# Kernel tuning notes

Measured on AMD Instinct MI355X. Metric: run time of the kernel, lower is better.

Reference implementation:

```python
import jax, jax.numpy as jnp
import numpy as np

N, M, D_IN, D_OUT = 100000, 1024, 64, 64


def setup_inputs() -> dict:
    key = jax.random.key(0)
    ks = jax.random.split(key, 8)
    # kaiming_uniform_ bound for fan_in = D_IN: sqrt(6 / fan_in) with a=sqrt(5) default? torch's
    # kaiming_uniform_ default (a=0) gives bound = sqrt(6/fan_in); exact init is irrelevant for math.
    bound = float(np.sqrt(6.0 / D_IN))
    return {
        "x": jax.random.normal(ks[0], (N, D_IN), dtype=jnp.float32),
        "neighbors": jax.random.normal(ks[1], (M, D_IN), dtype=jnp.float32),
        "Wq": jax.random.uniform(ks[2], (D_OUT, D_IN), jnp.float32, -bound, bound),
        "bq": jnp.zeros((D_OUT,), jnp.float32),
        "Wk": jax.random.uniform(ks[3], (D_OUT, D_IN), jnp.float32, -bound, bound),
        "bk": jnp.zeros((D_OUT,), jnp.float32),
        "Wv": jax.random.uniform(ks[4], (D_OUT, D_IN), jnp.float32, -bound, bound),
        "bv": jnp.zeros((D_OUT,), jnp.float32),
    }


def reference(x, neighbors, Wq, bq, Wk, bk, Wv, bv):
    # q: [N, D_OUT], k: [M, D_OUT]
    q = x @ Wq.T + bq
    k = neighbors @ Wk.T + bk
    # scores: [N, M] -- same math as sum(q[:,None,:] * k[None,:,:], axis=2) but via GEMM
    scores = q @ k.T
    attn = jax.nn.softmax(scores, axis=1)
    # attn @ neighbors: [N, D_IN], then value projection -> [N, D_OUT]
    agg = attn @ neighbors
    return agg @ Wv.T + bv
```

## Files before the change

### kernel.cpp

```cpp
#include <hip/hip_runtime.h>


#define N_ROWS 100000
#define VT_STRIDE 1040

typedef __attribute__((ext_vector_type(8))) _Float16 half8;
typedef __attribute__((ext_vector_type(4))) float    f32x4;

#define MFMA16(a,b,c) __builtin_amdgcn_mfma_f32_16x16x32_f16((a),(b),(c),0,0,0)

static __device__ __forceinline__ f32x4 zero4() {
    f32x4 v = {0.f, 0.f, 0.f, 0.f};
    return v;
}

__global__ __launch_bounds__(256)
void prep_kernel(const float* __restrict__ nb, const float* __restrict__ Wq,
                 const float* __restrict__ bq, const float* __restrict__ Wk,
                 unsigned short* __restrict__ Gh, unsigned short* __restrict__ Gl,
                 float* __restrict__ uW, unsigned short* __restrict__ Kp,
                 unsigned short* __restrict__ VTp)
{
    __shared__ __align__(16) float sm[8192];
    const int tid = threadIdx.x;
    if (blockIdx.x == 0) {
        const float4* wk4 = (const float4*)Wk;
        const float4* wq4 = (const float4*)Wq;
        float4* dk = (float4*)sm;
        float4* dq = (float4*)(sm + 4096);
        #pragma unroll
        for (int u = 0; u < 4; u++) {
            dk[u * 256 + tid] = wk4[u * 256 + tid];
            dq[u * 256 + tid] = wq4[u * 256 + tid];
        }
        __syncthreads();
        const int e2 = tid & 63, e1g = (tid >> 6) * 16;
        float g[16];
        #pragma unroll
        for (int q = 0; q < 16; q++) g[q] = 0.f;
        for (int w = 0; w < 64; w++) {
            float kv = sm[w * 64 + e2];
            const float* wqp = sm + 4096 + w * 64 + e1g;
            #pragma unroll
            for (int q = 0; q < 16; q++) g[q] = fmaf(wqp[q], kv, g[q]);
        }
        union { half8 h; uint4 u; } ph0, pl0, ph1, pl1;
        #pragma unroll
        for (int i = 0; i < 8; i++) {
            _Float16 h0 = (_Float16)g[i];
            ph0.h[i] = h0; pl0.h[i] = (_Float16)(g[i] - (float)h0);
            _Float16 h1 = (_Float16)g[8 + i];
            ph1.h[i] = h1; pl1.h[i] = (_Float16)(g[8 + i] - (float)h1);
        }
        *(uint4*)(Gh + e2 * 72 + e1g)     = ph0.u;
        *(uint4*)(Gh + e2 * 72 + e1g + 8) = ph1.u;
        *(uint4*)(Gl + e2 * 72 + e1g)     = pl0.u;
        *(uint4*)(Gl + e2 * 72 + e1g + 8) = pl1.u;
        if (tid < 64) {
            float uu = 0.f;
            for (int w = 0; w < 64; w++) uu = fmaf(bq[w], sm[w * 64 + tid], uu);
            uW[tid] = uu;
        }
    } else {
        const int j0 = (blockIdx.x - 1) * 64;
        const int jr = tid >> 2;
        const int c0 = (tid & 3) * 16;
        const float* np = nb + (size_t)(j0 + jr) * 64 + c0;
        float a[16];
        #pragma unroll
        for (int u = 0; u < 4; u++) *(float4*)(a + 4 * u) = *(const float4*)(np + 4 * u);
        const int pr = (jr & ~31) | (((jr >> 2) & 1) << 4) | (((jr >> 3) & 3) << 2) | (jr & 3);
        union { half8 h; uint4 u; } pk0, pk1;
        #pragma unroll
        for (int i = 0; i < 8; i++) { pk0.h[i] = (_Float16)a[i]; pk1.h[i] = (_Float16)a[8 + i]; }
        *(uint4*)(Kp + (size_t)(j0 + pr) * 72 + c0)     = pk0.u;
        *(uint4*)(Kp + (size_t)(j0 + pr) * 72 + c0 + 8) = pk1.u;
        #pragma unroll
        for (int i = 0; i < 16; i++) sm[jr * 65 + c0 + i] = a[i];
        __syncthreads();
        const int d   = tid >> 2;
        const int jc0 = (tid & 3) * 16;
        union { half8 h; uint4 u; } pv0, pv1;
        #pragma unroll
        for (int i = 0; i < 8; i++) {
            pv0.h[i] = (_Float16)sm[(jc0 + i) * 65 + d];
            pv1.h[i] = (_Float16)sm[(jc0 + 8 + i) * 65 + d];
        }
        *(uint4*)(VTp + (size_t)d * VT_STRIDE + j0 + jc0)     = pv0.u;
        *(uint4*)(VTp + (size_t)d * VT_STRIDE + j0 + jc0 + 8) = pv1.u;
    }
}

static __device__ __forceinline__ void flash_step(
    int jb, int jn, int c, int Q,
    const unsigned short* __restrict__ Kp, const unsigned short* __restrict__ VTp,
    const half8 (&ck0)[2], const half8 (&ck1)[2],
    half8 (&nk0)[2], half8 (&nk1)[2],
    const half8 (&qh)[2][2], const half8 (&ql)[2][2],
    f32x4 (&acc)[2][4], float (&mrow)[2], float (&lrow)[2])
{
    half8 vA[4];
    #pragma unroll
    for (int dt = 0; dt < 4; dt++)
        vA[dt] = *(const half8*)(VTp + (size_t)(dt * 16 + c) * VT_STRIDE + jb + Q * 8);
    #pragma unroll
    for (int t = 0; t < 2; t++) {
        const unsigned short* kp = Kp + (size_t)(jn + 16 * t + c) * 72;
        nk0[t] = *(const half8*)(kp + Q * 8);
        nk1[t] = *(const half8*)(kp + 32 + Q * 8);
    }
    f32x4 S[2][2];
    #pragma unroll
    for (int t = 0; t < 2; t++)
        #pragma unroll
        for (int qt = 0; qt < 2; qt++) {
            f32x4 s = MFMA16(ck0[t], qh[qt][0], zero4());
            s = MFMA16(ck1[t], qh[qt][1], s);
            s = MFMA16(ck0[t], ql[qt][0], s);
            s = MFMA16(ck1[t], ql[qt][1], s);
            S[t][qt] = s;
        }
    half8 pB[2];
    #pragma unroll
    for (int qt = 0; qt < 2; qt++) {
        float pmax = fmaxf(fmaxf(fmaxf(S[0][qt][0], S[0][qt][1]),
                                 fmaxf(S[0][qt][2], S[0][qt][3])),
                           fmaxf(fmaxf(S[1][qt][0], S[1][qt][1]),
                                 fmaxf(S[1][qt][2], S[1][qt][3])));
        if (__any(pmax > mrow[qt] + 8.f)) {
            float cm = pmax;
            cm = fmaxf(cm, __shfl_xor(cm, 16));
            cm = fmaxf(cm, __shfl_xor(cm, 32));
            const float mn = fmaxf(mrow[qt], cm);
            const float sc = __expf(mrow[qt] - mn);
            mrow[qt] = mn;
            lrow[qt] *= sc;
            #pragma unroll
            for (int dt = 0; dt < 4; dt++)
                #pragma unroll
                for (int r = 0; r < 4; r++) acc[qt][dt][r] *= sc;
        }
        const float mref = mrow[qt];
        float p[8]; float ps = 0.f;
        #pragma unroll
        for (int r = 0; r < 4; r++) { p[r] = __expf(S[0][qt][r] - mref); ps += p[r]; }
        #pragma unroll
        for (int r = 0; r < 4; r++) { p[4 + r] = __expf(S[1][qt][r] - mref); ps += p[4 + r]; }
        lrow[qt] += ps;
        #pragma unroll
        for (int i = 0; i < 8; i++) pB[qt][i] = (_Float16)p[i];
    }
    #pragma unroll
    for (int dt = 0; dt < 4; dt++) {
        acc[0][dt] = MFMA16(vA[dt], pB[0], acc[0][dt]);
        acc[1][dt] = MFMA16(vA[dt], pB[1], acc[1][dt]);
    }
}

__global__ __launch_bounds__(64, 3)
void attn_kernel(const float* __restrict__ x,
                 const unsigned short* __restrict__ Gh,
                 const unsigned short* __restrict__ Gl,
                 const float* __restrict__ uW,
                 const unsigned short* __restrict__ Kp,
                 const unsigned short* __restrict__ VTp,
                 const float* __restrict__ Wv,
                 const float* __restrict__ bv,
                 float* __restrict__ out)
{
    __shared__ __align__(16) float slice[1088];
    const int lane = threadIdx.x & 63;
    const int Q    = lane >> 4;
    const int c    = lane & 15;
    const int rbase = blockIdx.x * 32;

    half8 qh[2][2], ql[2][2];
    #pragma unroll
    for (int rt = 0; rt < 2; rt++) {
        int row = rbase + rt * 16 + c;
        if (row > N_ROWS - 1) row = N_ROWS - 1;
        half8 xh[2], xl[2];
        #pragma unroll
        for (int ks = 0; ks < 2; ks++) {
            const float* xp = x + (size_t)row * 64 + ks * 32 + Q * 8;
            float a[8];
            *(float4*)a       = *(const float4*)xp;
            *(float4*)(a + 4) = *(const float4*)(xp + 4);
            #pragma unroll
            for (int i = 0; i < 8; i++) {
                _Float16 h = (_Float16)a[i];
                xh[ks][i] = h;
                xl[ks][i] = (_Float16)(a[i] - (float)h);
            }
        }
        #pragma unroll
        for (int mt = 0; mt < 4; mt++) {
            f32x4 Cm = zero4();
            #pragma unroll
            for (int ks = 0; ks < 2; ks++) {
                half8 gh = *(const half8*)(Gh + (mt * 16 + c) * 72 + ks * 32 + Q * 8);
                half8 gl = *(const half8*)(Gl + (mt * 16 + c) * 72 + ks * 32 + Q * 8);
                Cm = MFMA16(gh, xh[ks], Cm);
                Cm = MFMA16(gh, xl[ks], Cm);
                Cm = MFMA16(gl, xh[ks], Cm);
            }
            *(f32x4*)(slice + c * 68 + mt * 16 + 4 * Q) = Cm;
        }
        __builtin_amdgcn_s_waitcnt(0);
        #pragma unroll
        for (int ks = 0; ks < 2; ks++) {
            const float* qp = slice + c * 68 + ks * 32 + Q * 8;
            const float* up = uW + ks * 32 + Q * 8;
            #pragma unroll
            for (int i = 0; i < 8; i++) {
                float val = qp[i] + up[i];
                _Float16 h = (_Float16)val;
                qh[rt][ks][i] = h;
                ql[rt][ks][i] = (_Float16)(val - (float)h);
            }
        }
        __builtin_amdgcn_s_waitcnt(0);
    }

    f32x4 acc[2][4];
    #pragma unroll
    for (int qt = 0; qt < 2; qt++)
        #pragma unroll
        for (int dt = 0; dt < 4; dt++) acc[qt][dt] = zero4();
    float mrow[2] = { -3.0e38f, -3.0e38f };
    float lrow[2] = { 0.f, 0.f };

    half8 ka0[2], ka1[2], kb0[2], kb1[2];
    #pragma unroll
    for (int t = 0; t < 2; t++) {
        const unsigned short* kp = Kp + (size_t)(16 * t + c) * 72;
        ka0[t] = *(const half8*)(kp + Q * 8);
        ka1[t] = *(const half8*)(kp + 32 + Q * 8);
    }
    #pragma unroll 1
    for (int jj = 0; jj < 16; jj++) {
        const int jb = jj * 64;
        flash_step(jb,      jb + 32, c, Q, Kp, VTp, ka0, ka1, kb0, kb1, qh, ql, acc, mrow, lrow);
        const int jn2 = (jb + 64 < 1024) ? jb + 64 : jb + 32;
        flash_step(jb + 32, jn2,     c, Q, Kp, VTp, kb0, kb1, ka0, ka1, qh, ql, acc, mrow, lrow);
    }

    #pragma unroll
    for (int qt = 0; qt < 2; qt++) {
        float l = lrow[qt];
        l += __shfl_xor(l, 16);
        l += __shfl_xor(l, 32);
        const float rl = 1.f / l;
        #pragma unroll
        for (int dt = 0; dt < 4; dt++)
            #pragma unroll
            for (int r = 0; r < 4; r++) acc[qt][dt][r] *= rl;
    }
    half8 wf[4][2];
    #pragma unroll
    for (int mt = 0; mt < 4; mt++)
        #pragma unroll
        for (int ks = 0; ks < 2; ks++) {
            const float* wp = Wv + (size_t)(mt * 16 + c) * 64 + ks * 32 + Q * 8;
            #pragma unroll
            for (int i = 0; i < 8; i++) wf[mt][ks][i] = (_Float16)wp[i];
        }
    const int srcA = 32 * (Q & 1) + c;
    const int srcB = srcA + 16;
    const bool hi = (Q >> 1) & 1;
    f32x4 o[2][4];
    #pragma unroll
    for (int qt = 0; qt < 2; qt++) {
        half8 pe[2];
        #pragma unroll
        for (int ks = 0; ks < 2; ks++) {
            #pragma unroll
            for (int r = 0; r < 4; r++) {
                float a0 = __shfl(acc[qt][2 * ks + 0][r], srcA);
                float a1 = __shfl(acc[qt][2 * ks + 1][r], srcA);
                float b0 = __shfl(acc[qt][2 * ks + 0][r], srcB);
                float b1 = __shfl(acc[qt][2 * ks + 1][r], srcB);
                pe[ks][r]     = (_Float16)(hi ? a1 : a0);
                pe[ks][4 + r] = (_Float16)(hi ? b1 : b0);
            }
        }
        #pragma unroll
        for (int mt = 0; mt < 4; mt++) {
            f32x4 t = MFMA16(wf[mt][0], pe[0], zero4());
            o[qt][mt] = MFMA16(wf[mt][1], pe[1], t);
        }
    }
    float4 bf[4];
    #pragma unroll
    for (int mt = 0; mt < 4; mt++) bf[mt] = *(const float4*)(bv + mt * 16 + 4 * Q);
    #pragma unroll
    for (int qt = 0; qt < 2; qt++) {
        const int row = rbase + qt * 16 + c;
        if (row < N_ROWS) {
            #pragma unroll
            for (int mt = 0; mt < 4; mt++) {
                float4 vv = make_float4(o[qt][mt][0] + bf[mt].x, o[qt][mt][1] + bf[mt].y,
                                        o[qt][mt][2] + bf[mt].z, o[qt][mt][3] + bf[mt].w);
                *(float4*)(out + (size_t)row * 64 + mt * 16 + 4 * Q) = vv;
            }
        }
    }
}

extern "C" void kernel_launch(void* const* d_in, const int* in_sizes, int n_in,
                              void* d_out, int out_size, void* d_ws, size_t ws_size,
                              hipStream_t stream)
{
    const float* x  = (const float*)d_in[0];
    const float* nb = (const float*)d_in[1];
    const float* Wq = (const float*)d_in[2];
    const float* bq = (const float*)d_in[3];
    const float* Wk = (const float*)d_in[4];
    const float* Wv = (const float*)d_in[6];
    const float* bv = (const float*)d_in[7];
    float* out = (float*)d_out;

    char* ws = (char*)d_ws;
    unsigned short* Gh  = (unsigned short*)(ws);
    unsigned short* Gl  = (unsigned short*)(ws + 9216);
    float*          uW  = (float*)(ws + 18432);
    unsigned short* Kp  = (unsigned short*)(ws + 18688);
    unsigned short* VTp = (unsigned short*)(ws + 166144);

    prep_kernel<<<17, 256, 0, stream>>>(nb, Wq, bq, Wk, Gh, Gl, uW, Kp, VTp);
    const int grid = N_ROWS / 32;
    attn_kernel<<<grid, 64, 0, stream>>>(x, Gh, Gl, uW, Kp, VTp, Wv, bv, out);
}
```

Baseline: 161.7 us.

## Pre-swizzle K, V and G into MFMA fragment order and prefetch V one tile ahead

After: 149.2 us. 1.08x faster.

```diff
diff --git a/kernel.cpp b/kernel.cpp
--- a/kernel.cpp
+++ b/kernel.cpp
@@ -2,7 +2,6 @@
 
 
 #define N_ROWS 100000
-#define VT_STRIDE 1040
 
 typedef __attribute__((ext_vector_type(8))) _Float16 half8;
 typedef __attribute__((ext_vector_type(4))) float    f32x4;
@@ -17,9 +16,9 @@
 __global__ __launch_bounds__(256)
 void prep_kernel(const float* __restrict__ nb, const float* __restrict__ Wq,
                  const float* __restrict__ bq, const float* __restrict__ Wk,
-                 unsigned short* __restrict__ Gh, unsigned short* __restrict__ Gl,
-                 float* __restrict__ uW, unsigned short* __restrict__ Kp,
-                 unsigned short* __restrict__ VTp)
+                 unsigned short* __restrict__ GFh, unsigned short* __restrict__ GFl,
+                 float* __restrict__ uW, unsigned short* __restrict__ KF,
+                 unsigned short* __restrict__ VF)
 {
     __shared__ __align__(16) float sm[8192];
     const int tid = threadIdx.x;
@@ -52,10 +51,13 @@
             _Float16 h1 = (_Float16)g[8 + i];
             ph1.h[i] = h1; pl1.h[i] = (_Float16)(g[8 + i] - (float)h1);
         }
-        *(uint4*)(Gh + e2 * 72 + e1g)     = ph0.u;
-        *(uint4*)(Gh + e2 * 72 + e1g + 8) = ph1.u;
-        *(uint4*)(Gl + e2 * 72 + e1g)     = pl0.u;
-        *(uint4*)(Gl + e2 * 72 + e1g + 8) = pl1.u;
+        const int mt = e2 >> 4, cc = e2 & 15;
+        const int ks = tid >> 7, Q0 = 2 * ((tid >> 6) & 1);
+        const int f  = mt * 2 + ks;
+        *(uint4*)(GFh + (f * 64 + Q0 * 16 + cc) * 8)       = ph0.u;
+        *(uint4*)(GFh + (f * 64 + (Q0 + 1) * 16 + cc) * 8) = ph1.u;
+        *(uint4*)(GFl + (f * 64 + Q0 * 16 + cc) * 8)       = pl0.u;
+        *(uint4*)(GFl + (f * 64 + (Q0 + 1) * 16 + cc) * 8) = pl1.u;
         if (tid < 64) {
             float uu = 0.f;
             for (int w = 0; w < 64; w++) uu = fmaf(bq[w], sm[w * 64 + tid], uu);
@@ -63,61 +65,69 @@
         }
     } else {
         const int j0 = (blockIdx.x - 1) * 64;
-        const int jr = tid >> 2;
-        const int c0 = (tid & 3) * 16;
-        const float* np = nb + (size_t)(j0 + jr) * 64 + c0;
-        float a[16];
-        #pragma unroll
-        for (int u = 0; u < 4; u++) *(float4*)(a + 4 * u) = *(const float4*)(np + 4 * u);
-        const int pr = (jr & ~31) | (((jr >> 2) & 1) << 4) | (((jr >> 3) & 3) << 2) | (jr & 3);
-        union { half8 h; uint4 u; } pk0, pk1;
-        #pragma unroll
-        for (int i = 0; i < 8; i++) { pk0.h[i] = (_Float16)a[i]; pk1.h[i] = (_Float16)a[8 + i]; }
-        *(uint4*)(Kp + (size_t)(j0 + pr) * 72 + c0)     = pk0.u;
-        *(uint4*)(Kp + (size_t)(j0 + pr) * 72 + c0 + 8) = pk1.u;
-        #pragma unroll
-        for (int i = 0; i < 16; i++) sm[jr * 65 + c0 + i] = a[i];
+        const int T0 = (blockIdx.x - 1) * 2;
+        {
+            const int jr = tid >> 2, c0 = (tid & 3) * 16;
+            const float* np = nb + (size_t)(j0 + jr) * 64 + c0;
+            #pragma unroll
+            for (int u = 0; u < 4; u++) {
+                float4 v = *(const float4*)(np + 4 * u);
+                sm[jr * 65 + c0 + 4 * u]     = v.x;
+                sm[jr * 65 + c0 + 4 * u + 1] = v.y;
+                sm[jr * 65 + c0 + 4 * u + 2] = v.z;
+                sm[jr * 65 + c0 + 4 * u + 3] = v.w;
+            }
+        }
+        #pragma unroll
+        for (int s = 0; s < 2; s++) {
+            const int slot = tid + 256 * s;
+            const int tt = (slot >> 8) & 1, f = (slot >> 6) & 3, ln = slot & 63;
+            const int t = f >> 1, h = f & 1, Qw = ln >> 4, cw = ln & 15;
+            const int key = ((cw >> 3) & 1) * 16 + ((cw >> 2) & 1) * 8 + 4 * t + (cw & 3);
+            const float* kp = nb + (size_t)((T0 + tt) * 32 + key) * 64 + h * 32 + Qw * 8;
+            float b[8];
+            *(float4*)b       = *(const float4*)kp;
+            *(float4*)(b + 4) = *(const float4*)(kp + 4);
+            union { half8 hh; uint4 u; } pk;
+            #pragma unroll
+            for (int i = 0; i < 8; i++) pk.hh[i] = (_Float16)b[i];
+            *(uint4*)(KF + (size_t)(T0 + tt) * 2048 + f * 512 + ln * 8) = pk.u;
+        }
         __syncthreads();
-        const int d   = tid >> 2;
-        const int jc0 = (tid & 3) * 16;
-        union { half8 h; uint4 u; } pv0, pv1;
-        #pragma unroll
-        for (int i = 0; i < 8; i++) {
-            pv0.h[i] = (_Float16)sm[(jc0 + i) * 65 + d];
-            pv1.h[i] = (_Float16)sm[(jc0 + 8 + i) * 65 + d];
-        }
-        *(uint4*)(VTp + (size_t)d * VT_STRIDE + j0 + jc0)     = pv0.u;
-        *(uint4*)(VTp + (size_t)d * VT_STRIDE + j0 + jc0 + 8) = pv1.u;
+        #pragma unroll
+        for (int s = 0; s < 2; s++) {
+            const int slot = tid + 256 * s;
+            const int tt = (slot >> 8) & 1, dt = (slot >> 6) & 3, ln = slot & 63;
+            const int Qw = ln >> 4, cw = ln & 15;
+            union { half8 hh; uint4 u; } pv;
+            #pragma unroll
+            for (int i = 0; i < 8; i++)
+                pv.hh[i] = (_Float16)sm[(tt * 32 + Qw * 8 + i) * 65 + dt * 16 + cw];
+            *(uint4*)(VF + (size_t)(T0 + tt) * 2048 + dt * 512 + ln * 8) = pv.u;
+        }
     }
 }
 
 static __device__ __forceinline__ void flash_step(
-    int jb, int jn, int c, int Q,
-    const unsigned short* __restrict__ Kp, const unsigned short* __restrict__ VTp,
-    const half8 (&ck0)[2], const half8 (&ck1)[2],
-    half8 (&nk0)[2], half8 (&nk1)[2],
+    const unsigned short* __restrict__ kfl, const unsigned short* __restrict__ vfl,
+    int Tn,
+    const half8 (&ck)[4], half8 (&nk)[4], half8 (&vA)[4],
     const half8 (&qh)[2][2], const half8 (&ql)[2][2],
     f32x4 (&acc)[2][4], float (&mrow)[2], float (&lrow)[2])
 {
-    half8 vA[4];
-    #pragma unroll
-    for (int dt = 0; dt < 4; dt++)
-        vA[dt] = *(const half8*)(VTp + (size_t)(dt * 16 + c) * VT_STRIDE + jb + Q * 8);
-    #pragma unroll
-    for (int t = 0; t < 2; t++) {
-        const unsigned short* kp = Kp + (size_t)(jn + 16 * t + c) * 72;
-        nk0[t] = *(const half8*)(kp + Q * 8);
-        nk1[t] = *(const half8*)(kp + 32 + Q * 8);
-    }
+    const unsigned short* kn = kfl + Tn * 2048;
+    #pragma unroll
+    for (int f = 0; f < 4; f++) nk[f] = *(const half8*)(kn + f * 512);
+
     f32x4 S[2][2];
     #pragma unroll
     for (int t = 0; t < 2; t++)
         #pragma unroll
         for (int qt = 0; qt < 2; qt++) {
-            f32x4 s = MFMA16(ck0[t], qh[qt][0], zero4());
-            s = MFMA16(ck1[t], qh[qt][1], s);
-            s = MFMA16(ck0[t], ql[qt][0], s);
-            s = MFMA16(ck1[t], ql[qt][1], s);
+            f32x4 s = MFMA16(ck[2 * t],     qh[qt][0], zero4());
+            s = MFMA16(ck[2 * t + 1], qh[qt][1], s);
+            s = MFMA16(ck[2 * t],     ql[qt][0], s);
+            s = MFMA16(ck[2 * t + 1], ql[qt][1], s);
             S[t][qt] = s;
         }
     half8 pB[2];
@@ -155,15 +165,18 @@
         acc[0][dt] = MFMA16(vA[dt], pB[0], acc[0][dt]);
         acc[1][dt] = MFMA16(vA[dt], pB[1], acc[1][dt]);
     }
+    const unsigned short* vn = vfl + Tn * 2048;
+    #pragma unroll
+    for (int d = 0; d < 4; d++) vA[d] = *(const half8*)(vn + d * 512);
 }
 
 __global__ __launch_bounds__(64, 3)
 void attn_kernel(const float* __restrict__ x,
-                 const unsigned short* __restrict__ Gh,
-                 const unsigned short* __restrict__ Gl,
+                 const unsigned short* __restrict__ GFh,
+                 const unsigned short* __restrict__ GFl,
                  const float* __restrict__ uW,
-                 const unsigned short* __restrict__ Kp,
-                 const unsigned short* __restrict__ VTp,
+                 const unsigned short* __restrict__ KF,
+                 const unsigned short* __restrict__ VF,
                  const float* __restrict__ Wv,
                  const float* __restrict__ bv,
                  float* __restrict__ out)
@@ -198,8 +211,8 @@
             f32x4 Cm = zero4();
             #pragma unroll
             for (int ks = 0; ks < 2; ks++) {
-                half8 gh = *(const half8*)(Gh + (mt * 16 + c) * 72 + ks * 32 + Q * 8);
-                half8 gl = *(const half8*)(Gl + (mt * 16 + c) * 72 + ks * 32 + Q * 8);
+                half8 gh = *(const half8*)(GFh + ((mt * 2 + ks) * 64 + lane) * 8);
+                half8 gl = *(const half8*)(GFl + ((mt * 2 + ks) * 64 + lane) * 8);
                 Cm = MFMA16(gh, xh[ks], Cm);
                 Cm = MFMA16(gh, xl[ks], Cm);
                 Cm = MFMA16(gl, xh[ks], Cm);
@@ -230,19 +243,19 @@
     float mrow[2] = { -3.0e38f, -3.0e38f };
     float lrow[2] = { 0.f, 0.f };
 
-    half8 ka0[2], ka1[2], kb0[2], kb1[2];
-    #pragma unroll
-    for (int t = 0; t < 2; t++) {
-        const unsigned short* kp = Kp + (size_t)(16 * t + c) * 72;
-        ka0[t] = *(const half8*)(kp + Q * 8);
-        ka1[t] = *(const half8*)(kp + 32 + Q * 8);
-    }
+    const unsigned short* kfl = KF + lane * 8;
+    const unsigned short* vfl = VF + lane * 8;
+    half8 kA[4], kB[4], vA[4];
+    #pragma unroll
+    for (int f = 0; f < 4; f++) kA[f] = *(const half8*)(kfl + f * 512);
+    #pragma unroll
+    for (int d = 0; d < 4; d++) vA[d] = *(const half8*)(vfl + d * 512);
+
     #pragma unroll 1
-    for (int jj = 0; jj < 16; jj++) {
-        const int jb = jj * 64;
-        flash_step(jb,      jb + 32, c, Q, Kp, VTp, ka0, ka1, kb0, kb1, qh, ql, acc, mrow, lrow);
-        const int jn2 = (jb + 64 < 1024) ? jb + 64 : jb + 32;
-        flash_step(jb + 32, jn2,     c, Q, Kp, VTp, kb0, kb1, ka0, ka1, qh, ql, acc, mrow, lrow);
+    for (int TT = 0; TT < 16; TT++) {
+        flash_step(kfl, vfl, 2 * TT + 1, kA, kB, vA, qh, ql, acc, mrow, lrow);
+        const int Tn = (2 * TT + 2 < 32) ? 2 * TT + 2 : 31;
+        flash_step(kfl, vfl, Tn,         kB, kA, vA, qh, ql, acc, mrow, lrow);
     }
 
     #pragma unroll
@@ -321,13 +334,13 @@
     float* out = (float*)d_out;
 
     char* ws = (char*)d_ws;
-    unsigned short* Gh  = (unsigned short*)(ws);
-    unsigned short* Gl  = (unsigned short*)(ws + 9216);
-    float*          uW  = (float*)(ws + 18432);
-    unsigned short* Kp  = (unsigned short*)(ws + 18688);
-    unsigned short* VTp = (unsigned short*)(ws + 166144);
-
-    prep_kernel<<<17, 256, 0, stream>>>(nb, Wq, bq, Wk, Gh, Gl, uW, Kp, VTp);
+    unsigned short* GFh = (unsigned short*)(ws);
+    unsigned short* GFl = (unsigned short*)(ws + 8192);
+    float*          uW  = (float*)(ws + 16384);
+    unsigned short* KF  = (unsigned short*)(ws + 16640);
+    unsigned short* VF  = (unsigned short*)(ws + 147712);
+
+    prep_kernel<<<17, 256, 0, stream>>>(nb, Wq, bq, Wk, GFh, GFl, uW, KF, VF);
     const int grid = N_ROWS / 32;
-    attn_kernel<<<grid, 64, 0, stream>>>(x, Gh, Gl, uW, Kp, VTp, Wv, bv, out);
-}
+    attn_kernel<<<grid, 64, 0, stream>>>(x, GFh, GFl, uW, KF, VF, Wv, bv, out);
+}
```
